# Optimization experiments

Measured on AMD Instinct MI355X. Metric: run time of the kernel, lower is better.

## Reference

```python
import jax, jax.numpy as jnp
import numpy as np

N_NODES = 40000
N_EDGES = 640000
IN_C = 128
HID = 32
HEADS = 4
OUT_C = 8
NUM_GRAPHS = 64
NEG_SLOPE = 0.2


def setup_inputs() -> dict:
    key = jax.random.key(0)
    ks = jax.random.split(key, 16)
    x = jax.random.normal(ks[0], (N_NODES, IN_C), dtype=jnp.float32)
    edge_index = jax.random.randint(ks[1], (2, N_EDGES), 0, N_NODES, dtype=jnp.int64)
    batch = jnp.sort(jax.random.randint(ks[2], (N_NODES,), 0, NUM_GRAPHS, dtype=jnp.int64))
    s = lambda k, shape, fan_in: jax.random.normal(k, shape, jnp.float32) / np.sqrt(fan_in)
    # conv0: in -> hid, 4 heads, concat
    W0 = s(ks[3], (IN_C, HEADS * HID), IN_C)
    a_src0 = s(ks[4], (HEADS, HID), HID)
    a_dst0 = s(ks[5], (HEADS, HID), HID)
    b0 = jnp.zeros((HEADS * HID,), jnp.float32)
    # conv1: hid*H -> hid, 4 heads, concat
    W1 = s(ks[6], (HEADS * HID, HEADS * HID), HEADS * HID)
    a_src1 = s(ks[7], (HEADS, HID), HID)
    a_dst1 = s(ks[8], (HEADS, HID), HID)
    b1 = jnp.zeros((HEADS * HID,), jnp.float32)
    # conv2: hid*H -> hid, 1 head, no concat
    W2 = s(ks[9], (HEADS * HID, HID), HEADS * HID)
    a_src2 = s(ks[10], (1, HID), HID)
    a_dst2 = s(ks[11], (1, HID), HID)
    b2 = jnp.zeros((HID,), jnp.float32)
    lin1_w = s(ks[12], (HID, IN_C), HID)
    lin1_b = jnp.zeros((IN_C,), jnp.float32)
    lin2_w = s(ks[13], (IN_C, OUT_C), IN_C)
    lin2_b = jnp.zeros((OUT_C,), jnp.float32)
    return dict(x=x, edge_index=edge_index, batch=batch,
                W0=W0, a_src0=a_src0, a_dst0=a_dst0, b0=b0,
                W1=W1, a_src1=a_src1, a_dst1=a_dst1, b1=b1,
                W2=W2, a_src2=a_src2, a_dst2=a_dst2, b2=b2,
                lin1_w=lin1_w, lin1_b=lin1_b, lin2_w=lin2_w, lin2_b=lin2_b)


def gat_conv(x, src, dst, W, a_src, a_dst, b, heads, out_c, concat):
    N = x.shape[0]
    h = (x @ W).reshape(N, heads, out_c)          # [N,H,C]
    als = (h * a_src[None]).sum(-1)               # [N,H]
    ald = (h * a_dst[None]).sum(-1)               # [N,H]
    e = jax.nn.leaky_relu(als[src] + ald[dst], NEG_SLOPE)  # [E,H]
    m = jax.ops.segment_max(e, dst, num_segments=N)
    m = jnp.where(jnp.isfinite(m), m, 0.0)
    p = jnp.exp(e - m[dst])                       # [E,H]
    denom = jax.ops.segment_sum(p, dst, num_segments=N)
    alpha = p / jnp.maximum(denom[dst], 1e-16)
    out = jax.ops.segment_sum(h[src] * alpha[:, :, None], dst, num_segments=N)
    out = out.reshape(N, heads * out_c) if concat else out.mean(axis=1)
    return out + b


def reference(x, edge_index, batch,
              W0, a_src0, a_dst0, b0,
              W1, a_src1, a_dst1, b1,
              W2, a_src2, a_dst2, b2,
              lin1_w, lin1_b, lin2_w, lin2_b):
    N = x.shape[0]
    # PyG GATConv adds self-loops by default
    loop = jnp.arange(N, dtype=edge_index.dtype)
    src = jnp.concatenate([edge_index[0], loop])
    dst = jnp.concatenate([edge_index[1], loop])
    # eval mode: dropout is identity
    h = jax.nn.elu(gat_conv(x, src, dst, W0, a_src0, a_dst0, b0, HEADS, HID, True))
    h = jax.nn.elu(gat_conv(h, src, dst, W1, a_src1, a_dst1, b1, HEADS, HID, True))
    h = jax.nn.elu(gat_conv(h, src, dst, W2, a_src2, a_dst2, b2, 1, HID, False))
    # global mean pool over graphs
    sums = jax.ops.segment_sum(h, batch, num_segments=NUM_GRAPHS)
    cnts = jax.ops.segment_sum(jnp.ones((N, 1), h.dtype), batch, num_segments=NUM_GRAPHS)
    g = sums / jnp.maximum(cnts, 1.0)             # [G, HID]
    g = jax.nn.relu(g @ lin1_w + lin1_b)
    return g @ lin2_w + lin2_b                    # [G, OUT_C]
```

## Files before the change

kernel.cpp:

```cpp
#include <hip/hip_runtime.h>
#include <hip/hip_bf16.h>

#define N_NODES 40000
#define N_EDGES 640000
#define E_TOT   (N_EDGES + N_NODES)
#define NUM_GRAPHS 64
#define CAP_SHIFT 6

#define CVTX_BLOCKS 5000
#define CVTW_BLOCKS 144
#define CVT_BLOCKS (CVTX_BLOCKS + CVTW_BLOCKS)
#define EBLOCKS ((E_TOT + 255) / 256)
#define GEMM_BLOCKS 625
#define NPHASE 5

typedef __attribute__((ext_vector_type(8))) short bf16x8;
typedef __attribute__((ext_vector_type(4))) float f32x4;

__device__ inline float bf2f(unsigned short u) {
    union { unsigned int i; float f; } v; v.i = ((unsigned int)u) << 16; return v.f;
}
__device__ inline unsigned short f2bf(float f) {
    union { float f; unsigned int i; } v; v.f = f;
    unsigned int r = v.i + 0x7FFF + ((v.i >> 16) & 1);
    return (unsigned short)(r >> 16);
}


__global__ __launch_bounds__(256) void cvt_scatter_kernel(const float* __restrict__ x,
                                                          const float* __restrict__ W0,
                                                          const float* __restrict__ W1,
                                                          const float* __restrict__ W2,
                                                          unsigned short* __restrict__ Xb,
                                                          unsigned short* __restrict__ Wt0,
                                                          unsigned short* __restrict__ Wt1,
                                                          unsigned short* __restrict__ Wt2,
                                                          const int* __restrict__ esrc,
                                                          const int* __restrict__ edst,
                                                          int* __restrict__ cnt,
                                                          unsigned short* __restrict__ psrc) {
    int b = blockIdx.x;
    int tid = threadIdx.x;
    if (b < CVTX_BLOCKS) {
        int i = b * 256 + tid;
        float4 v = ((const float4*)x)[i];
        ushort4 o;
        o.x = f2bf(v.x); o.y = f2bf(v.y); o.z = f2bf(v.z); o.w = f2bf(v.w);
        ((ushort4*)Xb)[i] = o;
    } else if (b < CVT_BLOCKS) {
        int idx = (b - CVTX_BLOCKS) * 256 + tid;
        if (idx < 16384) {
            int n = idx >> 7, k = idx & 127;
            Wt0[idx] = f2bf(W0[k * 128 + n]);
        } else if (idx < 32768) {
            int i = idx - 16384;
            int n = i >> 7, k = i & 127;
            Wt1[i] = f2bf(W1[k * 128 + n]);
        } else if (idx < 36864) {
            int i = idx - 32768;
            int n = i >> 7, k = i & 127;
            Wt2[i] = f2bf(W2[k * 32 + n]);
        }
    } else {
        int e = (b - CVT_BLOCKS) * 256 + tid;
        int d = -1, s = 0;
        if (e < E_TOT) {
            if (e < N_EDGES) { d = edst[e]; s = esrc[e]; }
            else             { d = e - N_EDGES; s = d; }
        }
#pragma unroll
        for (int p = 0; p < NPHASE; ++p) {
            if (d >= 0 && (d >> 13) == p) {
                int slot = atomicAdd(&cnt[d], 1);
                psrc[(d << CAP_SHIFT) + slot] = (unsigned short)s;
            }
        }
    }
}


__device__ __forceinline__ void gemm128_body(int blk,
                                             const unsigned short* __restrict__ Xb,
                                             const unsigned short* __restrict__ Wt,
                                             const float* __restrict__ asrc,
                                             const float* __restrict__ adst,
                                             unsigned short* __restrict__ Hb,
                                             float* __restrict__ ALS4,
                                             float* __restrict__ ALD4) {
    int wave = threadIdx.x >> 6;
    int lane = threadIdx.x & 63;
    int l15 = lane & 15;
    int q = lane >> 4;
    int r0 = (blk * 4 + wave) * 16;

    f32x4 acc[8];
#pragma unroll
    for (int t = 0; t < 8; ++t) acc[t] = (f32x4){0.f, 0.f, 0.f, 0.f};

    float asv[8], adv[8];
#pragma unroll
    for (int t = 0; t < 8; ++t) {
        int c = t * 16 + l15;
        asv[t] = asrc[c];
        adv[t] = adst[c];
    }

    const unsigned short* xrow = Xb + (long)(r0 + l15) * 128 + q * 8;
    const unsigned short* wrow = Wt + (long)l15 * 128 + q * 8;
#pragma unroll
    for (int kt = 0; kt < 4; ++kt) {
        bf16x8 a = *(const bf16x8*)(xrow + kt * 32);
#pragma unroll
        for (int t = 0; t < 8; ++t) {
            bf16x8 b = *(const bf16x8*)(wrow + (long)t * 16 * 128 + kt * 32);
            acc[t] = __builtin_amdgcn_mfma_f32_16x16x32_bf16(a, b, acc[t], 0, 0, 0);
        }
    }

#pragma unroll
    for (int t = 0; t < 8; ++t)
#pragma unroll
        for (int i = 0; i < 4; ++i)
            Hb[(long)(r0 + q * 4 + i) * 128 + t * 16 + l15] = f2bf(acc[t][i]);

#pragma unroll
    for (int i = 0; i < 4; ++i) {
        float ps0 = acc[0][i] * asv[0] + acc[1][i] * asv[1];
        float ps1 = acc[2][i] * asv[2] + acc[3][i] * asv[3];
        float ps2 = acc[4][i] * asv[4] + acc[5][i] * asv[5];
        float ps3 = acc[6][i] * asv[6] + acc[7][i] * asv[7];
        float pd0 = acc[0][i] * adv[0] + acc[1][i] * adv[1];
        float pd1 = acc[2][i] * adv[2] + acc[3][i] * adv[3];
        float pd2 = acc[4][i] * adv[4] + acc[5][i] * adv[5];
        float pd3 = acc[6][i] * adv[6] + acc[7][i] * adv[7];
#pragma unroll
        for (int m = 1; m < 16; m <<= 1) {
            ps0 += __shfl_xor(ps0, m, 16); ps1 += __shfl_xor(ps1, m, 16);
            ps2 += __shfl_xor(ps2, m, 16); ps3 += __shfl_xor(ps3, m, 16);
            pd0 += __shfl_xor(pd0, m, 16); pd1 += __shfl_xor(pd1, m, 16);
            pd2 += __shfl_xor(pd2, m, 16); pd3 += __shfl_xor(pd3, m, 16);
        }
        int r = r0 + q * 4 + i;
        if (l15 < 4) {
            float v = (l15 == 0) ? ps0 : (l15 == 1) ? ps1 : (l15 == 2) ? ps2 : ps3;
            ALS4[r * 4 + l15] = v;
        } else if (l15 < 8) {
            int h = l15 - 4;
            float v = (h == 0) ? pd0 : (h == 1) ? pd1 : (h == 2) ? pd2 : pd3;
            ALD4[r * 4 + h] = v;
        }
    }
}

__global__ __launch_bounds__(256) void gemm128_mfma(const unsigned short* __restrict__ Xb,
                                                    const unsigned short* __restrict__ Wt,
                                                    const float* __restrict__ asrc,
                                                    const float* __restrict__ adst,
                                                    unsigned short* __restrict__ Hb,
                                                    float* __restrict__ ALS4,
                                                    float* __restrict__ ALD4) {
    gemm128_body(blockIdx.x, Xb, Wt, asrc, adst, Hb, ALS4, ALD4);
}

__global__ __launch_bounds__(256) void gemm32_mfma(const unsigned short* __restrict__ Xb,
                                                   const unsigned short* __restrict__ Wt2,
                                                   const float* __restrict__ asrc,
                                                   const float* __restrict__ adst,
                                                   unsigned short* __restrict__ H2b,
                                                   float* __restrict__ ALS,
                                                   float* __restrict__ ALD) {
    int wave = threadIdx.x >> 6;
    int lane = threadIdx.x & 63;
    int l15 = lane & 15;
    int q = lane >> 4;
    int r0 = (blockIdx.x * 4 + wave) * 16;

    f32x4 acc[2];
    acc[0] = (f32x4){0.f, 0.f, 0.f, 0.f};
    acc[1] = (f32x4){0.f, 0.f, 0.f, 0.f};

    const unsigned short* xrow = Xb + (long)(r0 + l15) * 128 + q * 8;
    const unsigned short* wrow = Wt2 + (long)l15 * 128 + q * 8;
#pragma unroll
    for (int kt = 0; kt < 4; ++kt) {
        bf16x8 a = *(const bf16x8*)(xrow + kt * 32);
#pragma unroll
        for (int t = 0; t < 2; ++t) {
            bf16x8 b = *(const bf16x8*)(wrow + (long)t * 16 * 128 + kt * 32);
            acc[t] = __builtin_amdgcn_mfma_f32_16x16x32_bf16(a, b, acc[t], 0, 0, 0);
        }
    }

    float as0 = asrc[l15], as1 = asrc[16 + l15];
    float ad0 = adst[l15], ad1 = adst[16 + l15];
#pragma unroll
    for (int t = 0; t < 2; ++t)
#pragma unroll
        for (int i = 0; i < 4; ++i)
            H2b[(long)(r0 + q * 4 + i) * 32 + t * 16 + l15] = f2bf(acc[t][i]);

#pragma unroll
    for (int i = 0; i < 4; ++i) {
        float ps = acc[0][i] * as0 + acc[1][i] * as1;
        float pd = acc[0][i] * ad0 + acc[1][i] * ad1;
#pragma unroll
        for (int m = 1; m < 16; m <<= 1) {
            ps += __shfl_xor(ps, m, 16);
            pd += __shfl_xor(pd, m, 16);
        }
        if (l15 == 0) {
            int r = r0 + q * 4 + i;
            ALS[r] = ps;
            ALD[r] = pd;
        }
    }
}

__global__ __launch_bounds__(256) void agg128(const unsigned short* __restrict__ Hb,
                                              const float* __restrict__ ALS4,
                                              const float* __restrict__ ALD4,
                                              const int* __restrict__ cnt,
                                              const unsigned short* __restrict__ psrc,
                                              const float* __restrict__ bias,
                                              unsigned short* __restrict__ OUTb) {
    int n = blockIdx.x * 4 + (threadIdx.x >> 6);
    n = __builtin_amdgcn_readfirstlane(n);
    if (n >= N_NODES) return;
    int lane = threadIdx.x & 63;
    int c = lane * 2;
    int head = lane >> 4;
    int e16 = lane & 15;
    float aldh = ALD4[n * 4 + head];
    int j0 = n << CAP_SHIFT;
    int j1 = j0 + __builtin_amdgcn_readfirstlane(cnt[n]);
    float a0 = 0.f, a1 = 0.f, dsum = 0.f;
    for (int jb = j0; jb < j1; jb += 16) {
        int j = jb + e16;
        int jc = (j < j1) ? j : (j1 - 1);
        int s = (int)psrc[jc];
        float e = ALS4[s * 4 + head] + aldh;
        e = (e > 0.f) ? e : 0.2f * e;
        float w = (j < j1) ? __expf(e) : 0.f;
        int st[16]; float wt[16];
#pragma unroll
        for (int t = 0; t < 16; ++t) {
            st[t] = __shfl(s, t, 16);
            wt[t] = __shfl(w, t, 16);
        }
        unsigned int hv[16];
#pragma unroll
        for (int t = 0; t < 16; ++t)
            hv[t] = *(const unsigned int*)(Hb + (long)st[t] * 128 + c);
#pragma unroll
        for (int t = 0; t < 16; ++t) {
            float h0 = bf2f((unsigned short)(hv[t] & 0xFFFF));
            float h1 = bf2f((unsigned short)(hv[t] >> 16));
            dsum += wt[t];
            a0 += wt[t] * h0;
            a1 += wt[t] * h1;
        }
    }
    float inv = 1.0f / dsum;
    float o0 = a0 * inv + bias[c];
    float o1 = a1 * inv + bias[c + 1];
    o0 = (o0 > 0.f) ? o0 : (__expf(o0) - 1.f);
    o1 = (o1 > 0.f) ? o1 : (__expf(o1) - 1.f);
    ushort2 ob; ob.x = f2bf(o0); ob.y = f2bf(o1);
    *(ushort2*)(OUTb + (long)n * 128 + c) = ob;
}

__global__ __launch_bounds__(256) void agg32(const unsigned short* __restrict__ H2b,
                                             const float* __restrict__ ALS,
                                             const float* __restrict__ ALD,
                                             const int* __restrict__ cnt,
                                             const unsigned short* __restrict__ psrc,
                                             const float* __restrict__ bias,
                                             float* __restrict__ OUT) {
    int wv = blockIdx.x * 4 + (threadIdx.x >> 6);
    int lane = threadIdx.x & 63;
    int col = lane & 31;
    int half = lane >> 5;
    int e16 = lane & 15;
    int n = wv * 2 + half;
    if (n >= N_NODES) return;
    float aldn = ALD[n];
    int j0 = n << CAP_SHIFT;
    int j1 = j0 + cnt[n];
    float a = 0.f, dsum = 0.f;
    for (int jb = j0; jb < j1; jb += 16) {
        int j = jb + e16;
        int jc = (j < j1) ? j : (j1 - 1);
        int s = (int)psrc[jc];
        float e = ALS[s] + aldn;
        e = (e > 0.f) ? e : 0.2f * e;
        float w = (j < j1) ? __expf(e) : 0.f;
        int st[16]; float wt[16];
#pragma unroll
        for (int t = 0; t < 16; ++t) {
            st[t] = __shfl(s, t, 16);
            wt[t] = __shfl(w, t, 16);
        }
        unsigned short hv[16];
#pragma unroll
        for (int t = 0; t < 16; ++t)
            hv[t] = H2b[st[t] * 32 + col];
#pragma unroll
        for (int t = 0; t < 16; ++t) {
            dsum += wt[t];
            a += wt[t] * bf2f(hv[t]);
        }
    }
    float o = a / dsum + bias[col];
    o = (o > 0.f) ? o : (__expf(o) - 1.f);
    OUT[n * 32 + col] = o;
}

__global__ __launch_bounds__(256) void pool_kernel(const float* __restrict__ H3,
                                                   const int* __restrict__ batch,
                                                   float* __restrict__ gsum,
                                                   float* __restrict__ gcnt) {
    const int CHUNK = 40;
    int gid = (blockIdx.x * 256 + threadIdx.x) >> 5;
    int c = threadIdx.x & 31;
    int n0 = gid * CHUNK;
    if (n0 >= N_NODES) return;
    int n1 = n0 + CHUNK;
    if (n1 > N_NODES) n1 = N_NODES;
    int cur = batch[n0];
    float acc = 0.f;
    int cnt = 0;
    for (int n = n0; n < n1; ++n) {
        int b = batch[n];
        if (b != cur) {
            atomicAdd(&gsum[cur * 32 + c], acc);
            if (c == 0) atomicAdd(&gcnt[cur], (float)cnt);
            cur = b; acc = 0.f; cnt = 0;
        }
        acc += H3[n * 32 + c];
        cnt++;
    }
    atomicAdd(&gsum[cur * 32 + c], acc);
    if (c == 0) atomicAdd(&gcnt[cur], (float)cnt);
}

__global__ __launch_bounds__(256) void mlp_kernel(const float* __restrict__ gsum,
                                                  const float* __restrict__ gcnt,
                                                  const float* __restrict__ l1w,
                                                  const float* __restrict__ l1b,
                                                  const float* __restrict__ l2w,
                                                  const float* __restrict__ l2b,
                                                  float* __restrict__ out) {
    __shared__ float g[NUM_GRAPHS * 32];
    __shared__ float t1[NUM_GRAPHS * 128];
    int tid = threadIdx.x;
    for (int i = tid; i < NUM_GRAPHS * 32; i += 256) {
        float c = gcnt[i >> 5];
        g[i] = gsum[i] / fmaxf(c, 1.0f);
    }
    __syncthreads();
    for (int i = tid; i < NUM_GRAPHS * 128; i += 256) {
        int r = i >> 7, j = i & 127;
        float a = l1b[j];
        for (int k = 0; k < 32; ++k) a += g[r * 32 + k] * l1w[k * 128 + j];
        t1[i] = fmaxf(a, 0.f);
    }
    __syncthreads();
    for (int i = tid; i < NUM_GRAPHS * 8; i += 256) {
        int r = i >> 3, j = i & 7;
        float a = l2b[j];
        for (int k = 0; k < 128; ++k) a += t1[r * 128 + k] * l2w[k * 8 + j];
        out[i] = a;
    }
}


extern "C" void kernel_launch(void* const* d_in, const int* in_sizes, int n_in,
                              void* d_out, int out_size, void* d_ws, size_t ws_size,
                              hipStream_t stream) {
    const float* x      = (const float*)d_in[0];
    const int*   eidx   = (const int*)d_in[1];
    const int*   batch  = (const int*)d_in[2];
    const float* W0     = (const float*)d_in[3];
    const float* asrc0  = (const float*)d_in[4];
    const float* adst0  = (const float*)d_in[5];
    const float* b0     = (const float*)d_in[6];
    const float* W1     = (const float*)d_in[7];
    const float* asrc1  = (const float*)d_in[8];
    const float* adst1  = (const float*)d_in[9];
    const float* b1     = (const float*)d_in[10];
    const float* W2     = (const float*)d_in[11];
    const float* asrc2  = (const float*)d_in[12];
    const float* adst2  = (const float*)d_in[13];
    const float* b2     = (const float*)d_in[14];
    const float* l1w    = (const float*)d_in[15];
    const float* l1b    = (const float*)d_in[16];
    const float* l2w    = (const float*)d_in[17];
    const float* l2b    = (const float*)d_in[18];
    float* out = (float*)d_out;

    const int* esrc = eidx;
    const int* edst = eidx + N_EDGES;

    float* ALS  = (float*)d_ws;
    float* ALD  = ALS + N_NODES * 4;
    float* h3   = ALD + N_NODES * 4;
    int* cnt    = (int*)(h3 + (long)N_NODES * 32);
    float* gsum = (float*)(cnt + N_NODES);
    float* gcnt = gsum + NUM_GRAPHS * 32;
    unsigned short* psrc = (unsigned short*)(gcnt + NUM_GRAPHS);
    uintptr_t p = (uintptr_t)(psrc + ((long)N_NODES << CAP_SHIFT));
    p = (p + 15) & ~(uintptr_t)15;
    unsigned short* Xb   = (unsigned short*)p;
    unsigned short* Hb   = Xb + (long)N_NODES * 128;
    unsigned short* OUTb = Hb + (long)N_NODES * 128;
    unsigned short* H2b  = OUTb + (long)N_NODES * 128;
    unsigned short* Wt0  = H2b + (long)N_NODES * 32;
    unsigned short* Wt1  = Wt0 + 128 * 128;
    unsigned short* Wt2  = Wt1 + 128 * 128;

    size_t zbytes = (size_t)(N_NODES + NUM_GRAPHS * 32 + NUM_GRAPHS) * 4;
    hipMemsetAsync(cnt, 0, zbytes, stream);

    cvt_scatter_kernel<<<CVT_BLOCKS + EBLOCKS, 256, 0, stream>>>(
        x, W0, W1, W2, Xb, Wt0, Wt1, Wt2, esrc, edst, cnt, psrc);

    gemm128_mfma<<<GEMM_BLOCKS, 256, 0, stream>>>(Xb, Wt0, asrc0, adst0, Hb, ALS, ALD);
    agg128<<<10000, 256, 0, stream>>>(Hb, ALS, ALD, cnt, psrc, b0, OUTb);

    gemm128_mfma<<<GEMM_BLOCKS, 256, 0, stream>>>(OUTb, Wt1, asrc1, adst1, Hb, ALS, ALD);
    agg128<<<10000, 256, 0, stream>>>(Hb, ALS, ALD, cnt, psrc, b1, OUTb);

    gemm32_mfma<<<GEMM_BLOCKS, 256, 0, stream>>>(OUTb, Wt2, asrc2, adst2, H2b, ALS, ALD);
    agg32<<<5000, 256, 0, stream>>>(H2b, ALS, ALD, cnt, psrc, b2, h3);

    pool_kernel<<<125, 256, 0, stream>>>(h3, batch, gsum, gcnt);
    mlp_kernel<<<1, 256, 0, stream>>>(gsum, gcnt, l1w, l1b, l2w, l2b, out);
}
```

Measured before the change: 294.9 us.

## Replace per-node atomic CSR scatter with two-pass shared-memory binning

Edge-to-CSR construction now runs in two passes. The first bins edges by destination block of 256 nodes, staging them in shared memory and flushing 16-entry groups with one global atomic per bin. The second pass, fused into the first GEMM launch, sorts each bin into per-node buckets in LDS and writes psrc and cnt contiguously. This removes hundreds of thousands of scattered global atomics and random 2-byte writes, and drops the memset of cnt. In exchange it adds a staging buffer, many block-wide barriers, and 64 serialized binning blocks inside the convert kernel; BIN_CAP and STG overflow are not checked.

```diff
diff --git a/kernel.cpp b/kernel.cpp
--- a/kernel.cpp
+++ b/kernel.cpp
@@ -1,5 +1,4 @@
 #include <hip/hip_runtime.h>
-#include <hip/hip_bf16.h>
 
 #define N_NODES 40000
 #define N_EDGES 640000
@@ -9,10 +8,14 @@
 
 #define CVTX_BLOCKS 5000
 #define CVTW_BLOCKS 144
-#define CVT_BLOCKS (CVTX_BLOCKS + CVTW_BLOCKS)
-#define EBLOCKS ((E_TOT + 255) / 256)
+#define ABLKS 64
 #define GEMM_BLOCKS 625
-#define NPHASE 5
+
+#define BINS 157
+#define BIN_CAP 5120
+#define STG 48
+#define AROUNDS ((N_EDGES + ABLKS*256 - 1) / (ABLKS*256))
+#define NIT ((BINS + 15) / 16)
 
 typedef __attribute__((ext_vector_type(8))) short bf16x8;
 typedef __attribute__((ext_vector_type(4))) float f32x4;
@@ -27,28 +30,108 @@
 }
 
 
-__global__ __launch_bounds__(256) void cvt_scatter_kernel(const float* __restrict__ x,
-                                                          const float* __restrict__ W0,
-                                                          const float* __restrict__ W1,
-                                                          const float* __restrict__ W2,
-                                                          unsigned short* __restrict__ Xb,
-                                                          unsigned short* __restrict__ Wt0,
-                                                          unsigned short* __restrict__ Wt1,
-                                                          unsigned short* __restrict__ Wt2,
-                                                          const int* __restrict__ esrc,
-                                                          const int* __restrict__ edst,
-                                                          int* __restrict__ cnt,
-                                                          unsigned short* __restrict__ psrc) {
+__device__ void binA_body(int ab, const int* __restrict__ esrc,
+                          const int* __restrict__ edst,
+                          int* __restrict__ bin_gcnt,
+                          unsigned int* __restrict__ bins) {
+    __shared__ unsigned int astg[BINS * STG];
+    __shared__ int abcnt[BINS];
+    __shared__ int agbase[BINS];
+    __shared__ int anf[BINS];
+    int tid = threadIdx.x;
+    for (int i = tid; i < BINS; i += 256) abcnt[i] = 0;
+    __syncthreads();
+    int g16 = tid >> 4;
+    int l16 = tid & 15;
+    for (int r = 0; r < AROUNDS; ++r) {
+        int e = (r * ABLKS + ab) * 256 + tid;
+        int bin = -1; unsigned int entry = 0;
+        if (e < N_EDGES) {
+            int d = edst[e], s = esrc[e];
+            bin = d >> 8;
+            entry = ((unsigned int)(d & 255) << 16) | (unsigned int)s;
+        }
+        if (bin >= 0) {
+            int pos = atomicAdd(&abcnt[bin], 1);
+            astg[bin * STG + pos] = entry;
+        }
+        __syncthreads();
+        if (tid < BINS) {
+            int tot = abcnt[tid];
+            int nf = tot >> 4;
+            anf[tid] = nf;
+            if (nf) agbase[tid] = atomicAdd(&bin_gcnt[tid], nf * 16);
+        }
+        __syncthreads();
+        unsigned int rent[NIT];
+#pragma unroll
+        for (int it = 0; it < NIT; ++it) {
+            int bn = it * 16 + g16;
+            if (bn < BINS) {
+                int nf = anf[bn];
+                if (nf) {
+                    int gb = agbase[bn];
+                    for (int g = 0; g < nf; ++g)
+                        bins[bn * BIN_CAP + gb + g * 16 + l16] = astg[bn * STG + g * 16 + l16];
+                }
+                int rem = abcnt[bn] - nf * 16;
+                rent[it] = (l16 < rem) ? astg[bn * STG + nf * 16 + l16] : 0u;
+            }
+        }
+        __syncthreads();
+#pragma unroll
+        for (int it = 0; it < NIT; ++it) {
+            int bn = it * 16 + g16;
+            if (bn < BINS) {
+                int rem = abcnt[bn] - anf[bn] * 16;
+                if (l16 < rem) astg[bn * STG + l16] = rent[it];
+            }
+        }
+        __syncthreads();
+        if (tid < BINS) abcnt[tid] -= anf[tid] * 16;
+        __syncthreads();
+    }
+    if (tid < BINS) {
+        int tot = abcnt[tid];
+        if (tot) agbase[tid] = atomicAdd(&bin_gcnt[tid], tot);
+    }
+    __syncthreads();
+#pragma unroll
+    for (int it = 0; it < NIT; ++it) {
+        int bn = it * 16 + g16;
+        if (bn < BINS) {
+            int tot = abcnt[bn];
+            if (l16 < tot)
+                bins[bn * BIN_CAP + agbase[bn] + l16] = astg[bn * STG + l16];
+        }
+    }
+}
+
+
+__global__ __launch_bounds__(256) void cvt_binA_kernel(const float* __restrict__ x,
+                                                       const float* __restrict__ W0,
+                                                       const float* __restrict__ W1,
+                                                       const float* __restrict__ W2,
+                                                       unsigned short* __restrict__ Xb,
+                                                       unsigned short* __restrict__ Wt0,
+                                                       unsigned short* __restrict__ Wt1,
+                                                       unsigned short* __restrict__ Wt2,
+                                                       const int* __restrict__ esrc,
+                                                       const int* __restrict__ edst,
+                                                       int* __restrict__ bin_gcnt,
+                                                       unsigned int* __restrict__ bins) {
     int b = blockIdx.x;
     int tid = threadIdx.x;
-    if (b < CVTX_BLOCKS) {
-        int i = b * 256 + tid;
+    if (b < ABLKS) {
+        binA_body(b, esrc, edst, bin_gcnt, bins);
+    } else if (b < ABLKS + CVTX_BLOCKS) {
+        int i = (b - ABLKS) * 256 + tid;
         float4 v = ((const float4*)x)[i];
         ushort4 o;
         o.x = f2bf(v.x); o.y = f2bf(v.y); o.z = f2bf(v.z); o.w = f2bf(v.w);
         ((ushort4*)Xb)[i] = o;
-    } else if (b < CVT_BLOCKS) {
-        int idx = (b - CVTX_BLOCKS) * 256 + tid;
+    } else {
+        int idx = (b - ABLKS - CVTX_BLOCKS) * 256 + tid;
         if (idx < 16384) {
             int n = idx >> 7, k = idx & 127;
             Wt0[idx] = f2bf(W0[k * 128 + n]);
@@ -61,21 +144,39 @@
             int n = i >> 7, k = i & 127;
             Wt2[i] = f2bf(W2[k * 32 + n]);
         }
-    } else {
-        int e = (b - CVT_BLOCKS) * 256 + tid;
-        int d = -1, s = 0;
-        if (e < E_TOT) {
-            if (e < N_EDGES) { d = edst[e]; s = esrc[e]; }
-            else             { d = e - N_EDGES; s = d; }
-        }
-#pragma unroll
-        for (int p = 0; p < NPHASE; ++p) {
-            if (d >= 0 && (d >> 13) == p) {
-                int slot = atomicAdd(&cnt[d], 1);
-                psrc[(d << CAP_SHIFT) + slot] = (unsigned short)s;
-            }
-        }
-    }
+    }
+}
+
+
+__device__ void binB_body(int bb, const int* __restrict__ bin_gcnt,
+                          const unsigned int* __restrict__ bins,
+                          int* __restrict__ cnt,
+                          unsigned short* __restrict__ psrc) {
+    __shared__ unsigned short lbuck[256 * 64];
+    __shared__ int lcnt[256];
+    int tid = threadIdx.x;
+    lcnt[tid] = 0;
+    __syncthreads();
+    int cntE = bin_gcnt[bb];
+    for (int i = tid; i < cntE; i += 256) {
+        unsigned int entry = bins[bb * BIN_CAP + i];
+        int dl = entry >> 16;
+        int pos = atomicAdd(&lcnt[dl], 1);
+        lbuck[dl * 64 + pos] = (unsigned short)(entry & 0xFFFFu);
+    }
+    __syncthreads();
+    int node = bb * 256 + tid;
+    if (node < N_NODES) {
+        int pos = lcnt[tid];
+        lbuck[tid * 64 + pos] = (unsigned short)node;
+        lcnt[tid] = pos + 1;
+    }
+    __syncthreads();
+    int base = bb * (256 * 64);
+    int lim = (bb == BINS - 1) ? ((N_NODES - bb * 256) * 64) : (256 * 64);
+    for (int i = tid; i < lim; i += 256)
+        psrc[base + i] = lbuck[i];
+    if (node < N_NODES) cnt[node] = lcnt[tid];
 }
 
 
@@ -149,6 +250,25 @@
             float v = (h == 0) ? pd0 : (h == 1) ? pd1 : (h == 2) ? pd2 : pd3;
             ALD4[r * 4 + h] = v;
         }
+    }
+}
+
+__global__ __launch_bounds__(256) void gemm0_binB_kernel(const unsigned short* __restrict__ Xb,
+                                                         const unsigned short* __restrict__ Wt,
+                                                         const float* __restrict__ asrc,
+                                                         const float* __restrict__ adst,
+                                                         unsigned short* __restrict__ Hb,
+                                                         float* __restrict__ ALS4,
+                                                         float* __restrict__ ALD4,
+                                                         const int* __restrict__ bin_gcnt,
+                                                         const unsigned int* __restrict__ bins,
+                                                         int* __restrict__ cnt,
+                                                         unsigned short* __restrict__ psrc) {
+    int b = blockIdx.x;
+    if (b < BINS) {
+        binB_body(b, bin_gcnt, bins, cnt, psrc);
+    } else {
+        gemm128_body(b - BINS, Xb, Wt, asrc, adst, Hb, ALS4, ALD4);
     }
 }
 
@@ -405,9 +525,11 @@
     float* ALD  = ALS + N_NODES * 4;
     float* h3   = ALD + N_NODES * 4;
     int* cnt    = (int*)(h3 + (long)N_NODES * 32);
-    float* gsum = (float*)(cnt + N_NODES);
+    int* bin_gcnt = cnt + N_NODES;
+    float* gsum = (float*)(bin_gcnt + BINS);
     float* gcnt = gsum + NUM_GRAPHS * 32;
-    unsigned short* psrc = (unsigned short*)(gcnt + NUM_GRAPHS);
+    unsigned int* bins = (unsigned int*)(gcnt + NUM_GRAPHS);
+    unsigned short* psrc = (unsigned short*)(bins + (long)BINS * BIN_CAP);
     uintptr_t p = (uintptr_t)(psrc + ((long)N_NODES << CAP_SHIFT));
     p = (p + 15) & ~(uintptr_t)15;
     unsigned short* Xb   = (unsigned short*)p;
@@ -418,13 +540,14 @@
     unsigned short* Wt1  = Wt0 + 128 * 128;
     unsigned short* Wt2  = Wt1 + 128 * 128;
 
-    size_t zbytes = (size_t)(N_NODES + NUM_GRAPHS * 32 + NUM_GRAPHS) * 4;
-    hipMemsetAsync(cnt, 0, zbytes, stream);
-
-    cvt_scatter_kernel<<<CVT_BLOCKS + EBLOCKS, 256, 0, stream>>>(
-        x, W0, W1, W2, Xb, Wt0, Wt1, Wt2, esrc, edst, cnt, psrc);
-
-    gemm128_mfma<<<GEMM_BLOCKS, 256, 0, stream>>>(Xb, Wt0, asrc0, adst0, Hb, ALS, ALD);
+    size_t zbytes = (size_t)(BINS + NUM_GRAPHS * 32 + NUM_GRAPHS) * 4;
+    hipMemsetAsync(bin_gcnt, 0, zbytes, stream);
+
+    cvt_binA_kernel<<<ABLKS + CVTX_BLOCKS + CVTW_BLOCKS, 256, 0, stream>>>(
+        x, W0, W1, W2, Xb, Wt0, Wt1, Wt2, esrc, edst, bin_gcnt, bins);
+
+    gemm0_binB_kernel<<<BINS + GEMM_BLOCKS, 256, 0, stream>>>(
+        Xb, Wt0, asrc0, adst0, Hb, ALS, ALD, bin_gcnt, bins, cnt, psrc);
     agg128<<<10000, 256, 0, stream>>>(Hb, ALS, ALD, cnt, psrc, b0, OUTb);
 
     gemm128_mfma<<<GEMM_BLOCKS, 256, 0, stream>>>(OUTb, Wt1, asrc1, adst1, Hb, ALS, ALD);
```

Result: slower. 365.3 us (+23.9%).
